# Kernel optimization log

Measured on AMD Instinct MI355X. Metric: run time of the kernel, lower is better.

The kernel has to match this reference:

```python
import jax, jax.numpy as jnp
import numpy as np

B, S, D, H = 4, 2048, 1024, 16
DH = D // H


def setup_inputs() -> dict:
    key = jax.random.key(0)
    ks = jax.random.split(key, 7)
    return {
        "Q": jax.random.normal(ks[0], (B, S, D), dtype=jnp.float32),
        "K": jax.random.normal(ks[1], (B, S, D), dtype=jnp.float32),
        "V": jax.random.normal(ks[2], (B, S, D), dtype=jnp.float32),
        "q_proj": jax.random.normal(ks[3], (D, D), dtype=jnp.float32),
        "k_proj": jax.random.normal(ks[4], (D, D), dtype=jnp.float32),
        "v_proj": jax.random.normal(ks[5], (D, D), dtype=jnp.float32),
        "output_proj": jax.random.normal(ks[6], (D, D), dtype=jnp.float32),
        "casual": 1,
    }


def reference(Q, K, V, q_proj, k_proj, v_proj, output_proj, casual):
    # projections: einsum('... a b, ... s b -> ... s a') == x @ W.T
    q = jnp.einsum('bsd,ad->bsa', Q, q_proj)
    k = jnp.einsum('bsd,ad->bsa', K, k_proj)
    v = jnp.einsum('bsd,ad->bsa', V, v_proj)
    # split heads: [B, S, H, DH]
    q = q.reshape(B, S, H, DH)
    k = k.reshape(B, S, H, DH)
    v = v.reshape(B, S, H, DH)
    # scores [B, H, Sq, Sk]
    scores = jnp.einsum('bqhd,bkhd->bhqk', q, k) / np.sqrt(DH).astype(np.float32)
    # causal mask: 0 on lower triangle, -inf above
    causal_mask = jnp.where(
        jnp.tril(jnp.ones((S, S), dtype=bool)), 0.0, -jnp.inf
    ).astype(scores.dtype)
    scores = scores + causal_mask
    attn = jax.nn.softmax(scores, axis=-1)
    # weighted values -> [B, Sq, H, DH] -> [B, Sq, D]
    out = jnp.einsum('bhqk,bkhd->bqhd', attn, v).reshape(B, S, D)
    # output projection: einsum('... a b, ... b -> ... a') == x @ W.T
    return jnp.einsum('bsd,ad->bsa', out, output_proj)
```

## Files before the change

### kernel.cpp

```cpp
#include <hip/hip_runtime.h>


typedef __attribute__((ext_vector_type(8))) _Float16 half8;
typedef __attribute__((ext_vector_type(4))) float f32x4;

#define DEVI static __device__ __forceinline__

static constexpr int cB = 4, cS = 2048, cD = 1024, cH = 16, cDH = 64;
static constexpr int cM = cB * cS;

DEVI unsigned short h2b(_Float16 h) { union { _Float16 f; unsigned short u; } x; x.f = h; return x.u; }

DEVI void async16(const void* g, void* l) {
#if defined(__HIP_DEVICE_COMPILE__)
  __builtin_amdgcn_global_load_lds((const __attribute__((address_space(1))) unsigned int*)g,
                                   (__attribute__((address_space(3))) unsigned int*)l, 16, 0, 0);
#endif
}

__global__ void split_f16_kernel(const float* __restrict__ in, unsigned short* __restrict__ hi,
                                 unsigned short* __restrict__ lo, int n) {
  int i = (blockIdx.x * blockDim.x + threadIdx.x) * 4;
  if (i >= n) return;
  float4 v = *(const float4*)(in + i);
  _Float16 h0 = (_Float16)v.x, h1 = (_Float16)v.y, h2 = (_Float16)v.z, h3 = (_Float16)v.w;
  unsigned short th[4] = {h2b(h0), h2b(h1), h2b(h2), h2b(h3)};
  *(uint2*)(hi + i) = *(const uint2*)th;
  if (lo != nullptr) {
    unsigned short tl[4] = {h2b((_Float16)(v.x - (float)h0)), h2b((_Float16)(v.y - (float)h1)),
                            h2b((_Float16)(v.z - (float)h2)), h2b((_Float16)(v.w - (float)h3))};
    *(uint2*)(lo + i) = *(const uint2*)tl;
  }
}

template <int PASSES, int OUTMODE, bool A32>
__global__ __launch_bounds__(256, 2) void gemm_bt(const void* __restrict__ Ap,
                                                  const unsigned short* __restrict__ Bh,
                                                  const unsigned short* __restrict__ Bl,
                                                  void* __restrict__ C0, void* __restrict__ C1,
                                                  int M, int N, int K) {
  __shared__ float sA32[A32 ? 128 * 32 : 1];
  __shared__ unsigned short sA16[A32 ? 1 : 128 * 32];
  __shared__ unsigned short sBh[128 * 32];
  __shared__ unsigned short sBl[(PASSES == 3) ? 128 * 32 : 1];

  const int tid = threadIdx.x, lane = tid & 63, wave = tid >> 6;
  const int wm = wave >> 1, wn = wave & 1;
  const int nb = N >> 7;
  const int bm = blockIdx.x / nb, bn = blockIdx.x % nb;
  const long r0 = (long)bm * 128, c0 = (long)bn * 128;
  const int quad = lane >> 4, cl = lane & 15;

  f32x4 acc[4][4];
#pragma unroll
  for (int mt = 0; mt < 4; ++mt)
#pragma unroll
    for (int nt = 0; nt < 4; ++nt) acc[mt][nt] = f32x4{0.f, 0.f, 0.f, 0.f};

  const int lrow8 = lane >> 3, lg8 = lane & 7;
  const int lrow16 = lane >> 2, lg4 = lane & 3;

  const float* A32p = (const float*)Ap;
  const unsigned short* A16p = (const unsigned short*)Ap;

  for (int k0 = 0; k0 < K; k0 += 32) {
    __syncthreads();
    if constexpr (A32) {
#pragma unroll
      for (int c = 0; c < 4; ++c) {
        int cc = wave * 4 + c;
        int r = cc * 8 + lrow8;
        const float* g = A32p + (r0 + r) * (long)K + k0 + ((lg8 ^ lrow8) * 4);
        async16(g, sA32 + cc * 256);
      }
    } else {
#pragma unroll
      for (int c = 0; c < 2; ++c) {
        int cc = wave * 2 + c;
        int r = cc * 16 + lrow16;
        const unsigned short* g =
            A16p + (r0 + r) * (long)K + k0 + ((lg4 ^ ((lrow16 >> 1) & 3)) * 8);
        async16(g, sA16 + cc * 512);
      }
    }
#pragma unroll
    for (int c = 0; c < 2; ++c) {
      int cc = wave * 2 + c;
      int r = cc * 16 + lrow16;
      long gb = (c0 + r) * (long)K + k0 + ((lg4 ^ ((lrow16 >> 1) & 3)) * 8);
      async16(Bh + gb, sBh + cc * 512);
      if constexpr (PASSES == 3) async16(Bl + gb, sBl + cc * 512);
    }
    __syncthreads();

    half8 ah[4], al[4], bh8[4], bl8[4];
    if constexpr (A32) {
#pragma unroll
      for (int mt = 0; mt < 4; ++mt) {
        int r = wm * 64 + mt * 16 + cl;
        int s0 = (quad * 2 + 0) ^ (r & 7), s1 = (quad * 2 + 1) ^ (r & 7);
        float fa[8];
        *(float4*)(fa) = *(const float4*)(sA32 + r * 32 + s0 * 4);
        *(float4*)(fa + 4) = *(const float4*)(sA32 + r * 32 + s1 * 4);
#pragma unroll
        for (int j = 0; j < 8; ++j) {
          _Float16 hh = (_Float16)fa[j];
          ah[mt][j] = hh;
          if constexpr (PASSES == 3) al[mt][j] = (_Float16)(fa[j] - (float)hh);
        }
      }
    } else {
#pragma unroll
      for (int mt = 0; mt < 4; ++mt) {
        int r = wm * 64 + mt * 16 + cl;
        int s = quad ^ ((r >> 1) & 3);
        ah[mt] = *(const half8*)(sA16 + r * 32 + s * 8);
      }
    }
#pragma unroll
    for (int nt = 0; nt < 4; ++nt) {
      int r = wn * 64 + nt * 16 + cl;
      int s = quad ^ ((r >> 1) & 3);
      bh8[nt] = *(const half8*)(sBh + r * 32 + s * 8);
      if constexpr (PASSES == 3) bl8[nt] = *(const half8*)(sBl + r * 32 + s * 8);
    }
#pragma unroll
    for (int mt = 0; mt < 4; ++mt)
#pragma unroll
      for (int nt = 0; nt < 4; ++nt) {
        acc[mt][nt] = __builtin_amdgcn_mfma_f32_16x16x32_f16(ah[mt], bh8[nt], acc[mt][nt], 0, 0, 0);
        if constexpr (PASSES == 3) {
          acc[mt][nt] = __builtin_amdgcn_mfma_f32_16x16x32_f16(ah[mt], bl8[nt], acc[mt][nt], 0, 0, 0);
          acc[mt][nt] = __builtin_amdgcn_mfma_f32_16x16x32_f16(al[mt], bh8[nt], acc[mt][nt], 0, 0, 0);
        }
      }
  }

#pragma unroll
  for (int mt = 0; mt < 4; ++mt)
#pragma unroll
    for (int nt = 0; nt < 4; ++nt)
#pragma unroll
      for (int i = 0; i < 4; ++i) {
        long row = r0 + wm * 64 + mt * 16 + quad * 4 + i;
        long col = c0 + wn * 64 + nt * 16 + cl;
        float v = acc[mt][nt][i];
        if constexpr (OUTMODE == 2) {
          ((float*)C0)[row * N + col] = v;
        } else if constexpr (OUTMODE == 0) {
          ((unsigned short*)C0)[row * N + col] = h2b((_Float16)v);
        } else {
          _Float16 hh = (_Float16)v;
          ((unsigned short*)C0)[row * N + col] = h2b(hh);
          ((unsigned short*)C1)[row * N + col] = h2b((_Float16)(v - (float)hh));
        }
      }
}

__global__ __launch_bounds__(256, 3) void flash_kernel(
    const unsigned short* __restrict__ qh_g, const unsigned short* __restrict__ ql_g,
    const unsigned short* __restrict__ kh_g, const unsigned short* __restrict__ kl_g,
    const unsigned short* __restrict__ vp_g, unsigned short* __restrict__ out) {
  __shared__ unsigned short sKh[64 * 64];
  __shared__ unsigned short sKl[64 * 64];
  __shared__ unsigned int sVtU[64 * 34];
  __shared__ unsigned short sP[4][32 * 40];

  const int tid = threadIdx.x, lane = tid & 63, wave = tid >> 6;
  const int quad = lane >> 4, cl = lane & 15;
  const int bh = blockIdx.x & 63;
  const int qt = 15 - (blockIdx.x >> 6);
  const int h = bh & 15;
  const int b = bh >> 4;
  const long rowbase = (long)b * cS;
  const int q0 = qt * 128;
  const int lrow8 = lane >> 3, lg8 = lane & 7;

  half8 qh[2][2], ql[2][2];
  const _Float16 s8 = (_Float16)0.125f;
#pragma unroll
  for (int ks = 0; ks < 2; ++ks)
#pragma unroll
    for (int mt = 0; mt < 2; ++mt) {
      long r = rowbase + q0 + wave * 32 + mt * 16 + cl;
      long off = r * cD + h * 64 + ks * 32 + quad * 8;
      qh[ks][mt] = *(const half8*)(qh_g + off) * s8;
      ql[ks][mt] = *(const half8*)(ql_g + off) * s8;
    }

  f32x4 O[2][5];
  float mrow[2][4];
#pragma unroll
  for (int mt = 0; mt < 2; ++mt) {
#pragma unroll
    for (int dt = 0; dt < 5; ++dt) O[mt][dt] = f32x4{0.f, 0.f, 0.f, 0.f};
#pragma unroll
    for (int i = 0; i < 4; ++i) mrow[mt][i] = -1e30f;
  }

  half8 vone;
#pragma unroll
  for (int j = 0; j < 8; ++j) vone[j] = (cl == 0) ? (_Float16)1.0f : (_Float16)0.0f;

  auto tile = [&](int ki, bool MASK) {
    __syncthreads();
#pragma unroll
    for (int c = 0; c < 2; ++c) {
      int cc = wave * 2 + c;
      int r = cc * 8 + lrow8;
      long g = (rowbase + ki * 64 + r) * (long)cD + h * 64 + ((lg8 ^ lrow8) * 8);
      async16(kh_g + g, sKh + cc * 512);
      async16(kl_g + g, sKl + cc * 512);
    }
    {
      int r2 = tid & 31, dc = (tid >> 5) * 8;
      const unsigned short* gv = vp_g + (rowbase + ki * 64 + 2 * r2) * (long)cD + h * 64 + dc;
      unsigned short a[8], bb[8];
      *(uint4*)a = *(const uint4*)gv;
      *(uint4*)bb = *(const uint4*)(gv + cD);
#pragma unroll
      for (int j = 0; j < 8; ++j)
        sVtU[(dc + j) * 34 + r2] = (unsigned int)a[j] | ((unsigned int)bb[j] << 16);
    }
    __syncthreads();

    f32x4 sacc[2][4];
#pragma unroll
    for (int mt = 0; mt < 2; ++mt)
#pragma unroll
      for (int nt = 0; nt < 4; ++nt) sacc[mt][nt] = f32x4{0.f, 0.f, 0.f, 0.f};
#pragma unroll
    for (int ks = 0; ks < 2; ++ks) {
      half8 kh8[4], kl8[4];
#pragma unroll
      for (int nt = 0; nt < 4; ++nt) {
        int r = nt * 16 + cl;
        int off = r * 64 + (((ks * 4 + quad) ^ (r & 7)) * 8);
        kh8[nt] = *(const half8*)(sKh + off);
        kl8[nt] = *(const half8*)(sKl + off);
      }
#pragma unroll
      for (int mt = 0; mt < 2; ++mt)
#pragma unroll
        for (int nt = 0; nt < 4; ++nt) {
          sacc[mt][nt] = __builtin_amdgcn_mfma_f32_16x16x32_f16(qh[ks][mt], kh8[nt], sacc[mt][nt], 0, 0, 0);
          sacc[mt][nt] = __builtin_amdgcn_mfma_f32_16x16x32_f16(qh[ks][mt], kl8[nt], sacc[mt][nt], 0, 0, 0);
          sacc[mt][nt] = __builtin_amdgcn_mfma_f32_16x16x32_f16(ql[ks][mt], kh8[nt], sacc[mt][nt], 0, 0, 0);
        }
    }
    if (MASK) {
#pragma unroll
      for (int mt = 0; mt < 2; ++mt)
#pragma unroll
        for (int nt = 0; nt < 4; ++nt)
#pragma unroll
          for (int i = 0; i < 4; ++i) {
            int rg = q0 + wave * 32 + mt * 16 + quad * 4 + i;
            int cg = ki * 64 + nt * 16 + cl;
            if (cg > rg) sacc[mt][nt][i] = -1e30f;
          }
    }
    float mnew[2][4];
    bool ch = false;
#pragma unroll
    for (int mt = 0; mt < 2; ++mt)
#pragma unroll
      for (int i = 0; i < 4; ++i) {
        float mx = fmaxf(fmaxf(sacc[mt][0][i], sacc[mt][1][i]),
                         fmaxf(sacc[mt][2][i], sacc[mt][3][i]));
#pragma unroll
        for (int d = 1; d < 16; d <<= 1) mx = fmaxf(mx, __shfl_xor(mx, d));
        ch |= (mx > mrow[mt][i]);
        mnew[mt][i] = fmaxf(mrow[mt][i], mx);
      }
    if (__ballot(ch)) {
#pragma unroll
      for (int mt = 0; mt < 2; ++mt)
#pragma unroll
        for (int i = 0; i < 4; ++i) {
          float a = __expf(mrow[mt][i] - mnew[mt][i]);
#pragma unroll
          for (int dt = 0; dt < 5; ++dt) O[mt][dt][i] *= a;
        }
    }
#pragma unroll
    for (int mt = 0; mt < 2; ++mt)
#pragma unroll
      for (int i = 0; i < 4; ++i) mrow[mt][i] = mnew[mt][i];

    unsigned short* sPw = sP[wave];
#pragma unroll
    for (int kc = 0; kc < 2; ++kc) {
#pragma unroll
      for (int mt = 0; mt < 2; ++mt)
#pragma unroll
        for (int ntl = 0; ntl < 2; ++ntl) {
          int nt = kc * 2 + ntl;
#pragma unroll
          for (int i = 0; i < 4; ++i) {
            float p = __expf(sacc[mt][nt][i] - mrow[mt][i]);
            sPw[(mt * 16 + quad * 4 + i) * 40 + ntl * 16 + cl] = h2b((_Float16)p);
          }
        }
      half8 pa[2], vb[4];
#pragma unroll
      for (int mt = 0; mt < 2; ++mt)
        pa[mt] = *(const half8*)(sPw + (mt * 16 + cl) * 40 + quad * 8);
#pragma unroll
      for (int dt = 0; dt < 4; ++dt) {
        int base = (dt * 16 + cl) * 34 + kc * 16 + quad * 4;
        union { uint4 u; half8 hh; } cvt;
        uint2 p0 = *(const uint2*)(sVtU + base);
        uint2 p1 = *(const uint2*)(sVtU + base + 2);
        cvt.u = uint4{p0.x, p0.y, p1.x, p1.y};
        vb[dt] = cvt.hh;
      }
#pragma unroll
      for (int mt = 0; mt < 2; ++mt) {
#pragma unroll
        for (int dt = 0; dt < 4; ++dt)
          O[mt][dt] = __builtin_amdgcn_mfma_f32_16x16x32_f16(pa[mt], vb[dt], O[mt][dt], 0, 0, 0);
        O[mt][4] = __builtin_amdgcn_mfma_f32_16x16x32_f16(pa[mt], vone, O[mt][4], 0, 0, 0);
      }
    }
  };

  const int full = 2 * qt;
  for (int ki = 0; ki < full; ++ki) tile(ki, false);
  tile(full, true);
  tile(full + 1, true);

  float lv[2][4];
#pragma unroll
  for (int mt = 0; mt < 2; ++mt)
#pragma unroll
    for (int i = 0; i < 4; ++i) lv[mt][i] = __shfl(O[mt][4][i], (lane & 48));
#pragma unroll
  for (int mt = 0; mt < 2; ++mt)
#pragma unroll
    for (int dt = 0; dt < 4; ++dt)
#pragma unroll
      for (int i = 0; i < 4; ++i) {
        long r = rowbase + q0 + wave * 32 + mt * 16 + quad * 4 + i;
        out[r * cD + h * 64 + dt * 16 + cl] = h2b((_Float16)(O[mt][dt][i] / lv[mt][i]));
      }
}

extern "C" void kernel_launch(void* const* d_in, const int* in_sizes, int n_in,
                              void* d_out, int out_size, void* d_ws, size_t ws_size,
                              hipStream_t stream) {
  const float* Q = (const float*)d_in[0];
  const float* K = (const float*)d_in[1];
  const float* V = (const float*)d_in[2];
  const float* Wq = (const float*)d_in[3];
  const float* Wk = (const float*)d_in[4];
  const float* Wv = (const float*)d_in[5];
  const float* Wo = (const float*)d_in[6];

  unsigned short* ws = (unsigned short*)d_ws;
  const size_t WD = (size_t)cD * cD;
  const size_t WM = (size_t)cM * cD;
  unsigned short* Wqh = ws;
  unsigned short* Wql = Wqh + WD;
  unsigned short* Wkh = Wql + WD;
  unsigned short* Wkl = Wkh + WD;
  unsigned short* Wvh = Wkl + WD;
  unsigned short* Woh = Wvh + WD;
  unsigned short* qph = Woh + WD;
  unsigned short* qpl = qph + WM;
  unsigned short* kph = qpl + WM;
  unsigned short* kpl = kph + WM;
  unsigned short* vp = kpl + WM;
  unsigned short* attnb = vp + WM;

  const int nW = (int)WD;
  split_f16_kernel<<<nW / 1024, 256, 0, stream>>>(Wq, Wqh, Wql, nW);
  split_f16_kernel<<<nW / 1024, 256, 0, stream>>>(Wk, Wkh, Wkl, nW);
  split_f16_kernel<<<nW / 1024, 256, 0, stream>>>(Wv, Wvh, nullptr, nW);
  split_f16_kernel<<<nW / 1024, 256, 0, stream>>>(Wo, Woh, nullptr, nW);

  const int gblk = (cM / 128) * (cD / 128);
  gemm_bt<3, 1, true><<<gblk, 256, 0, stream>>>(Q, Wqh, Wql, qph, qpl, cM, cD, cD);
  gemm_bt<3, 1, true><<<gblk, 256, 0, stream>>>(K, Wkh, Wkl, kph, kpl, cM, cD, cD);
  gemm_bt<1, 0, true><<<gblk, 256, 0, stream>>>(V, Wvh, nullptr, vp, nullptr, cM, cD, cD);

  flash_kernel<<<cB * cH * 16, 256, 0, stream>>>(qph, qpl, kph, kpl, vp, attnb);

  gemm_bt<1, 2, false><<<gblk, 256, 0, stream>>>(attnb, Woh, nullptr, d_out, nullptr, cM, cD, cD);
}
```

Measured before the change: 490.0 us.

## Prefetch next K/V tile during current tile's compute in attention loop

Restructures the attention key loop into a software pipeline. The next tile's async K load into LDS and its V global load into registers are issued right after the current K fragments have been pulled into registers. This is meant to hide global memory latency behind the second QK half, the softmax and the PV MFMAs. It costs extra V registers (double-buffered uint4 pairs), and the mask flag becomes a runtime check instead of a separately specialised call.

```diff
diff --git a/kernel.cpp b/kernel.cpp
--- a/kernel.cpp
+++ b/kernel.cpp
@@ -202,8 +202,13 @@
 #pragma unroll
   for (int j = 0; j < 8; ++j) vone[j] = (cl == 0) ? (_Float16)1.0f : (_Float16)0.0f;
 
-  auto tile = [&](int ki, bool MASK) {
-    __syncthreads();
+  const int r2 = tid & 31, dc = (tid >> 5) * 8;
+  const unsigned short* vtile0 = vp_g + (rowbase + 2 * r2) * (long)cD + h * 64 + dc;
+
+  const int full = 2 * qt;
+  const int NT = full + 2;
+
+  auto stageK = [&](int ki) {
 #pragma unroll
     for (int c = 0; c < 2; ++c) {
       int cc = wave * 2 + c;
@@ -212,42 +217,75 @@
       async16(kh_g + g, sKh + cc * 512);
       async16(kl_g + g, sKl + cc * 512);
     }
+  };
+  auto loadV = [&](int ki, uint4& v0, uint4& v1) {
+    const unsigned short* gv = vtile0 + (long)ki * 64 * cD;
+    v0 = *(const uint4*)gv;
+    v1 = *(const uint4*)(gv + cD);
+  };
+
+  uint4 va0, va1, vb0, vb1;
+  stageK(0);
+  loadV(0, va0, va1);
+
+  auto body = [&](int ki, const uint4& cv0, const uint4& cv1, uint4& nv0, uint4& nv1) {
+    const bool MASK = ki >= full;
+    __syncthreads();
     {
-      int r2 = tid & 31, dc = (tid >> 5) * 8;
-      const unsigned short* gv = vp_g + (rowbase + ki * 64 + 2 * r2) * (long)cD + h * 64 + dc;
       unsigned short a[8], bb[8];
-      *(uint4*)a = *(const uint4*)gv;
-      *(uint4*)bb = *(const uint4*)(gv + cD);
+      *(uint4*)a = cv0;
+      *(uint4*)bb = cv1;
 #pragma unroll
       for (int j = 0; j < 8; ++j)
         sVtU[(dc + j) * 34 + r2] = (unsigned int)a[j] | ((unsigned int)bb[j] << 16);
     }
+
+    f32x4 sacc[2][4];
+#pragma unroll
+    for (int mt = 0; mt < 2; ++mt)
+#pragma unroll
+      for (int nt = 0; nt < 4; ++nt) sacc[mt][nt] = f32x4{0.f, 0.f, 0.f, 0.f};
+
+    half8 kh8[4], kl8[4];
+#pragma unroll
+    for (int nt = 0; nt < 4; ++nt) {
+      int r = nt * 16 + cl;
+      int off = r * 64 + ((quad ^ (r & 7)) * 8);
+      kh8[nt] = *(const half8*)(sKh + off);
+      kl8[nt] = *(const half8*)(sKl + off);
+    }
+#pragma unroll
+    for (int mt = 0; mt < 2; ++mt)
+#pragma unroll
+      for (int nt = 0; nt < 4; ++nt) {
+        sacc[mt][nt] = __builtin_amdgcn_mfma_f32_16x16x32_f16(qh[0][mt], kh8[nt], sacc[mt][nt], 0, 0, 0);
+        sacc[mt][nt] = __builtin_amdgcn_mfma_f32_16x16x32_f16(qh[0][mt], kl8[nt], sacc[mt][nt], 0, 0, 0);
+        sacc[mt][nt] = __builtin_amdgcn_mfma_f32_16x16x32_f16(ql[0][mt], kh8[nt], sacc[mt][nt], 0, 0, 0);
+      }
+    half8 kh8b[4], kl8b[4];
+#pragma unroll
+    for (int nt = 0; nt < 4; ++nt) {
+      int r = nt * 16 + cl;
+      int off = r * 64 + (((4 + quad) ^ (r & 7)) * 8);
+      kh8b[nt] = *(const half8*)(sKh + off);
+      kl8b[nt] = *(const half8*)(sKl + off);
+    }
+
     __syncthreads();
-
-    f32x4 sacc[2][4];
+    if (ki + 1 < NT) {
+      stageK(ki + 1);
+      loadV(ki + 1, nv0, nv1);
+    }
+
 #pragma unroll
     for (int mt = 0; mt < 2; ++mt)
 #pragma unroll
-      for (int nt = 0; nt < 4; ++nt) sacc[mt][nt] = f32x4{0.f, 0.f, 0.f, 0.f};
-#pragma unroll
-    for (int ks = 0; ks < 2; ++ks) {
-      half8 kh8[4], kl8[4];
-#pragma unroll
       for (int nt = 0; nt < 4; ++nt) {
-        int r = nt * 16 + cl;
-        int off = r * 64 + (((ks * 4 + quad) ^ (r & 7)) * 8);
-        kh8[nt] = *(const half8*)(sKh + off);
-        kl8[nt] = *(const half8*)(sKl + off);
-      }
-#pragma unroll
-      for (int mt = 0; mt < 2; ++mt)
-#pragma unroll
-        for (int nt = 0; nt < 4; ++nt) {
-          sacc[mt][nt] = __builtin_amdgcn_mfma_f32_16x16x32_f16(qh[ks][mt], kh8[nt], sacc[mt][nt], 0, 0, 0);
-          sacc[mt][nt] = __builtin_amdgcn_mfma_f32_16x16x32_f16(qh[ks][mt], kl8[nt], sacc[mt][nt], 0, 0, 0);
-          sacc[mt][nt] = __builtin_amdgcn_mfma_f32_16x16x32_f16(ql[ks][mt], kh8[nt], sacc[mt][nt], 0, 0, 0);
-        }
-    }
+        sacc[mt][nt] = __builtin_amdgcn_mfma_f32_16x16x32_f16(qh[1][mt], kh8b[nt], sacc[mt][nt], 0, 0, 0);
+        sacc[mt][nt] = __builtin_amdgcn_mfma_f32_16x16x32_f16(qh[1][mt], kl8b[nt], sacc[mt][nt], 0, 0, 0);
+        sacc[mt][nt] = __builtin_amdgcn_mfma_f32_16x16x32_f16(ql[1][mt], kh8b[nt], sacc[mt][nt], 0, 0, 0);
+      }
+
     if (MASK) {
 #pragma unroll
       for (int mt = 0; mt < 2; ++mt)
@@ -325,10 +363,10 @@
     }
   };
 
-  const int full = 2 * qt;
-  for (int ki = 0; ki < full; ++ki) tile(ki, false);
-  tile(full, true);
-  tile(full + 1, true);
+  for (int ki = 0; ki < NT; ki += 2) {
+    body(ki, va0, va1, vb0, vb1);
+    body(ki + 1, vb0, vb1, va0, va1);
+  }
 
   float lv[2][4];
 #pragma unroll
```

New measurement: 519.1 us. 5.9% more time.

## Merge weight splits and Q/K/V projection GEMMs into single launches

Applied to the files above, without the earlier changes.

Folds the four weight-splitting launches into one kernel indexed by block, and merges the three Q/K/V projection GEMMs into one grid of 1536 blocks that picks its job at runtime. Each projection block still runs its own job; the gain comes from fewer launches and better GPU fill across jobs, since each GEMM had only 512 blocks. The cost is runtime branching on p3 instead of compile-time templates, which may raise register and LDS use (the V job also allocates sBl) and change occupancy under the new launch bounds of 3. The output GEMM becomes a dedicated fp16-A kernel.

```diff
diff --git a/kernel.cpp b/kernel.cpp
--- a/kernel.cpp
+++ b/kernel.cpp
@@ -18,10 +18,16 @@
 #endif
 }
 
-__global__ void split_f16_kernel(const float* __restrict__ in, unsigned short* __restrict__ hi,
-                                 unsigned short* __restrict__ lo, int n) {
-  int i = (blockIdx.x * blockDim.x + threadIdx.x) * 4;
-  if (i >= n) return;
+__global__ void split4_kernel(const float* __restrict__ Wq, const float* __restrict__ Wk,
+                              const float* __restrict__ Wv, const float* __restrict__ Wo,
+                              unsigned short* __restrict__ Wqh, unsigned short* __restrict__ Wql,
+                              unsigned short* __restrict__ Wkh, unsigned short* __restrict__ Wkl,
+                              unsigned short* __restrict__ Wvh, unsigned short* __restrict__ Woh) {
+  const int w = blockIdx.x >> 10, blk = blockIdx.x & 1023;
+  const float* in = (w == 0) ? Wq : (w == 1) ? Wk : (w == 2) ? Wv : Wo;
+  unsigned short* hi = (w == 0) ? Wqh : (w == 1) ? Wkh : (w == 2) ? Wvh : Woh;
+  unsigned short* lo = (w == 0) ? Wql : (w == 1) ? Wkl : nullptr;
+  int i = (blk * 256 + (int)threadIdx.x) * 4;
   float4 v = *(const float4*)(in + i);
   _Float16 h0 = (_Float16)v.x, h1 = (_Float16)v.y, h2 = (_Float16)v.z, h3 = (_Float16)v.w;
   unsigned short th[4] = {h2b(h0), h2b(h1), h2b(h2), h2b(h3)};
@@ -33,16 +39,120 @@
   }
 }
 
-template <int PASSES, int OUTMODE, bool A32>
-__global__ __launch_bounds__(256, 2) void gemm_bt(const void* __restrict__ Ap,
-                                                  const unsigned short* __restrict__ Bh,
-                                                  const unsigned short* __restrict__ Bl,
-                                                  void* __restrict__ C0, void* __restrict__ C1,
-                                                  int M, int N, int K) {
-  __shared__ float sA32[A32 ? 128 * 32 : 1];
-  __shared__ unsigned short sA16[A32 ? 1 : 128 * 32];
+__global__ __launch_bounds__(256, 3) void proj_fused(
+    const float* __restrict__ Qa, const float* __restrict__ Ka, const float* __restrict__ Va,
+    const unsigned short* __restrict__ Wqh, const unsigned short* __restrict__ Wql,
+    const unsigned short* __restrict__ Wkh, const unsigned short* __restrict__ Wkl,
+    const unsigned short* __restrict__ Wvh,
+    unsigned short* __restrict__ qph, unsigned short* __restrict__ qpl,
+    unsigned short* __restrict__ kph, unsigned short* __restrict__ kpl,
+    unsigned short* __restrict__ vp) {
+  constexpr int N = cD, K = cD;
+  __shared__ float sA32[128 * 32];
   __shared__ unsigned short sBh[128 * 32];
-  __shared__ unsigned short sBl[(PASSES == 3) ? 128 * 32 : 1];
+  __shared__ unsigned short sBl[128 * 32];
+
+  const int job = blockIdx.x >> 9;
+  const int bid = blockIdx.x & 511;
+  const bool p3 = (job < 2);
+  const float* A32p = (job == 0) ? Qa : (job == 1) ? Ka : Va;
+  const unsigned short* Bh = (job == 0) ? Wqh : (job == 1) ? Wkh : Wvh;
+  const unsigned short* Bl = (job == 0) ? Wql : Wkl;
+  unsigned short* C0 = (job == 0) ? qph : (job == 1) ? kph : vp;
+  unsigned short* C1 = (job == 0) ? qpl : kpl;
+
+  const int tid = threadIdx.x, lane = tid & 63, wave = tid >> 6;
+  const int wm = wave >> 1, wn = wave & 1;
+  const int bm = bid >> 3, bn = bid & 7;
+  const long r0 = (long)bm * 128, c0 = (long)bn * 128;
+  const int quad = lane >> 4, cl = lane & 15;
+
+  f32x4 acc[4][4];
+#pragma unroll
+  for (int mt = 0; mt < 4; ++mt)
+#pragma unroll
+    for (int nt = 0; nt < 4; ++nt) acc[mt][nt] = f32x4{0.f, 0.f, 0.f, 0.f};
+
+  const int lrow8 = lane >> 3, lg8 = lane & 7;
+  const int lrow16 = lane >> 2, lg4 = lane & 3;
+
+  for (int k0 = 0; k0 < K; k0 += 32) {
+    __syncthreads();
+#pragma unroll
+    for (int c = 0; c < 4; ++c) {
+      int cc = wave * 4 + c;
+      int r = cc * 8 + lrow8;
+      const float* g = A32p + (r0 + r) * (long)K + k0 + ((lg8 ^ lrow8) * 4);
+      async16(g, sA32 + cc * 256);
+    }
+#pragma unroll
+    for (int c = 0; c < 2; ++c) {
+      int cc = wave * 2 + c;
+      int r = cc * 16 + lrow16;
+      long gb = (c0 + r) * (long)K + k0 + ((lg4 ^ ((lrow16 >> 1) & 3)) * 8);
+      async16(Bh + gb, sBh + cc * 512);
+      if (p3) async16(Bl + gb, sBl + cc * 512);
+    }
+    __syncthreads();
+
+    half8 ah[4], al[4], bh8[4], bl8[4];
+#pragma unroll
+    for (int mt = 0; mt < 4; ++mt) {
+      int r = wm * 64 + mt * 16 + cl;
+      int s0 = (quad * 2 + 0) ^ (r & 7), s1 = (quad * 2 + 1) ^ (r & 7);
+      float fa[8];
+      *(float4*)(fa) = *(const float4*)(sA32 + r * 32 + s0 * 4);
+      *(float4*)(fa + 4) = *(const float4*)(sA32 + r * 32 + s1 * 4);
+#pragma unroll
+      for (int j = 0; j < 8; ++j) {
+        _Float16 hh = (_Float16)fa[j];
+        ah[mt][j] = hh;
+        if (p3) al[mt][j] = (_Float16)(fa[j] - (float)hh);
+      }
+    }
+#pragma unroll
+    for (int nt = 0; nt < 4; ++nt) {
+      int r = wn * 64 + nt * 16 + cl;
+      int s = quad ^ ((r >> 1) & 3);
+      bh8[nt] = *(const half8*)(sBh + r * 32 + s * 8);
+      if (p3) bl8[nt] = *(const half8*)(sBl + r * 32 + s * 8);
+    }
+#pragma unroll
+    for (int mt = 0; mt < 4; ++mt)
+#pragma unroll
+      for (int nt = 0; nt < 4; ++nt) {
+        acc[mt][nt] = __builtin_amdgcn_mfma_f32_16x16x32_f16(ah[mt], bh8[nt], acc[mt][nt], 0, 0, 0);
+        if (p3) {
+          acc[mt][nt] = __builtin_amdgcn_mfma_f32_16x16x32_f16(ah[mt], bl8[nt], acc[mt][nt], 0, 0, 0);
+          acc[mt][nt] = __builtin_amdgcn_mfma_f32_16x16x32_f16(al[mt], bh8[nt], acc[mt][nt], 0, 0, 0);
+        }
+      }
+  }
+
+#pragma unroll
+  for (int mt = 0; mt < 4; ++mt)
+#pragma unroll
+    for (int nt = 0; nt < 4; ++nt)
+#pragma unroll
+      for (int i = 0; i < 4; ++i) {
+        long row = r0 + wm * 64 + mt * 16 + quad * 4 + i;
+        long col = c0 + wn * 64 + nt * 16 + cl;
+        float v = acc[mt][nt][i];
+        if (p3) {
+          _Float16 hh = (_Float16)v;
+          C0[row * N + col] = h2b(hh);
+          C1[row * N + col] = h2b((_Float16)(v - (float)hh));
+        } else {
+          C0[row * N + col] = h2b((_Float16)v);
+        }
+      }
+}
+
+__global__ __launch_bounds__(256, 2) void gemm_out(const unsigned short* __restrict__ A16p,
+                                                   const unsigned short* __restrict__ Bh,
+                                                   float* __restrict__ C0, int M, int N, int K) {
+  __shared__ unsigned short sA16[128 * 32];
+  __shared__ unsigned short sBh[128 * 32];
 
   const int tid = threadIdx.x, lane = tid & 63, wave = tid >> 6;
   const int wm = wave >> 1, wn = wave & 1;
@@ -57,83 +167,39 @@
 #pragma unroll
     for (int nt = 0; nt < 4; ++nt) acc[mt][nt] = f32x4{0.f, 0.f, 0.f, 0.f};
 
-  const int lrow8 = lane >> 3, lg8 = lane & 7;
   const int lrow16 = lane >> 2, lg4 = lane & 3;
 
-  const float* A32p = (const float*)Ap;
-  const unsigned short* A16p = (const unsigned short*)Ap;
-
   for (int k0 = 0; k0 < K; k0 += 32) {
     __syncthreads();
-    if constexpr (A32) {
-#pragma unroll
-      for (int c = 0; c < 4; ++c) {
-        int cc = wave * 4 + c;
-        int r = cc * 8 + lrow8;
-        const float* g = A32p + (r0 + r) * (long)K + k0 + ((lg8 ^ lrow8) * 4);
-        async16(g, sA32 + cc * 256);
-      }
-    } else {
-#pragma unroll
-      for (int c = 0; c < 2; ++c) {
-        int cc = wave * 2 + c;
-        int r = cc * 16 + lrow16;
-        const unsigned short* g =
-            A16p + (r0 + r) * (long)K + k0 + ((lg4 ^ ((lrow16 >> 1) & 3)) * 8);
-        async16(g, sA16 + cc * 512);
-      }
-    }
 #pragma unroll
     for (int c = 0; c < 2; ++c) {
       int cc = wave * 2 + c;
       int r = cc * 16 + lrow16;
+      long ga = (r0 + r) * (long)K + k0 + ((lg4 ^ ((lrow16 >> 1) & 3)) * 8);
+      async16(A16p + ga, sA16 + cc * 512);
       long gb = (c0 + r) * (long)K + k0 + ((lg4 ^ ((lrow16 >> 1) & 3)) * 8);
       async16(Bh + gb, sBh + cc * 512);
-      if constexpr (PASSES == 3) async16(Bl + gb, sBl + cc * 512);
-    }
-    __syncthreads();
-
-    half8 ah[4], al[4], bh8[4], bl8[4];
-    if constexpr (A32) {
-#pragma unroll
-      for (int mt = 0; mt < 4; ++mt) {
-        int r = wm * 64 + mt * 16 + cl;
-        int s0 = (quad * 2 + 0) ^ (r & 7), s1 = (quad * 2 + 1) ^ (r & 7);
-        float fa[8];
-        *(float4*)(fa) = *(const float4*)(sA32 + r * 32 + s0 * 4);
-        *(float4*)(fa + 4) = *(const float4*)(sA32 + r * 32 + s1 * 4);
-#pragma unroll
-        for (int j = 0; j < 8; ++j) {
-          _Float16 hh = (_Float16)fa[j];
-          ah[mt][j] = hh;
-          if constexpr (PASSES == 3) al[mt][j] = (_Float16)(fa[j] - (float)hh);
-        }
-      }
-    } else {
-#pragma unroll
-      for (int mt = 0; mt < 4; ++mt) {
-        int r = wm * 64 + mt * 16 + cl;
-        int s = quad ^ ((r >> 1) & 3);
-        ah[mt] = *(const half8*)(sA16 + r * 32 + s * 8);
-      }
+    }
+    __syncthreads();
+
+    half8 ah[4], bh8[4];
+#pragma unroll
+    for (int mt = 0; mt < 4; ++mt) {
+      int r = wm * 64 + mt * 16 + cl;
+      int s = quad ^ ((r >> 1) & 3);
+      ah[mt] = *(const half8*)(sA16 + r * 32 + s * 8);
     }
 #pragma unroll
     for (int nt = 0; nt < 4; ++nt) {
       int r = wn * 64 + nt * 16 + cl;
       int s = quad ^ ((r >> 1) & 3);
       bh8[nt] = *(const half8*)(sBh + r * 32 + s * 8);
-      if constexpr (PASSES == 3) bl8[nt] = *(const half8*)(sBl + r * 32 + s * 8);
     }
 #pragma unroll
     for (int mt = 0; mt < 4; ++mt)
 #pragma unroll
-      for (int nt = 0; nt < 4; ++nt) {
+      for (int nt = 0; nt < 4; ++nt)
         acc[mt][nt] = __builtin_amdgcn_mfma_f32_16x16x32_f16(ah[mt], bh8[nt], acc[mt][nt], 0, 0, 0);
-        if constexpr (PASSES == 3) {
-          acc[mt][nt] = __builtin_amdgcn_mfma_f32_16x16x32_f16(ah[mt], bl8[nt], acc[mt][nt], 0, 0, 0);
-          acc[mt][nt] = __builtin_amdgcn_mfma_f32_16x16x32_f16(al[mt], bh8[nt], acc[mt][nt], 0, 0, 0);
-        }
-      }
   }
 
 #pragma unroll
@@ -144,16 +210,7 @@
       for (int i = 0; i < 4; ++i) {
         long row = r0 + wm * 64 + mt * 16 + quad * 4 + i;
         long col = c0 + wn * 64 + nt * 16 + cl;
-        float v = acc[mt][nt][i];
-        if constexpr (OUTMODE == 2) {
-          ((float*)C0)[row * N + col] = v;
-        } else if constexpr (OUTMODE == 0) {
-          ((unsigned short*)C0)[row * N + col] = h2b((_Float16)v);
-        } else {
-          _Float16 hh = (_Float16)v;
-          ((unsigned short*)C0)[row * N + col] = h2b(hh);
-          ((unsigned short*)C1)[row * N + col] = h2b((_Float16)(v - (float)hh));
-        }
+        C0[row * N + col] = acc[mt][nt][i];
       }
 }
 
@@ -373,18 +430,13 @@
   unsigned short* vp = kpl + WM;
   unsigned short* attnb = vp + WM;
 
-  const int nW = (int)WD;
-  split_f16_kernel<<<nW / 1024, 256, 0, stream>>>(Wq, Wqh, Wql, nW);
-  split_f16_kernel<<<nW / 1024, 256, 0, stream>>>(Wk, Wkh, Wkl, nW);
-  split_f16_kernel<<<nW / 1024, 256, 0, stream>>>(Wv, Wvh, nullptr, nW);
-  split_f16_kernel<<<nW / 1024, 256, 0, stream>>>(Wo, Woh, nullptr, nW);
+  split4_kernel<<<4096, 256, 0, stream>>>(Wq, Wk, Wv, Wo, Wqh, Wql, Wkh, Wkl, Wvh, Woh);
+
+  proj_fused<<<1536, 256, 0, stream>>>(Q, K, V, Wqh, Wql, Wkh, Wkl, Wvh,
+                                       qph, qpl, kph, kpl, vp);
+
+  flash_kernel<<<cB * cH * 16, 256, 0, stream>>>(qph, qpl, kph, kpl, vp, attnb);
 
   const int gblk = (cM / 128) * (cD / 128);
-  gemm_bt<3, 1, true><<<gblk, 256, 0, stream>>>(Q, Wqh, Wql, qph, qpl, cM, cD, cD);
-  gemm_bt<3, 1, true><<<gblk, 256, 0, stream>>>(K, Wkh, Wkl, kph, kpl, cM, cD, cD);
-  gemm_bt<1, 0, true><<<gblk, 256, 0, stream>>>(V, Wvh, nullptr, vp, nullptr, cM, cD, cD);
-
-  flash_kernel<<<cB * cH * 16, 256, 0, stream>>>(qph, qpl, kph, kpl, vp, attnb);
-
-  gemm_bt<1, 2, false><<<gblk, 256, 0, stream>>>(attnb, Woh, nullptr, d_out, nullptr, cM, cD, cD);
-}
+  gemm_out<<<gblk, 256, 0, stream>>>(attnb, Woh, (float*)d_out, cM, cD, cD);
+}
```

After: 542.7 us. +10.7%, slower.
